# Performance work log

Hardware: AMD Instinct MI355X
Metric: run time of the kernel (lower is better)

Reference implementation:

```python
import jax, jax.numpy as jnp
import numpy as np
from jax import lax

V, E, H, N, To, Ti = 4000, 512, 512, 32, 128, 512
SOS_ID, EOS_ID = 1, 2


def setup_inputs() -> dict:
    key = jax.random.key(0)
    ks = jax.random.split(key, 16)
    s = 0.05
    inp = {}
    inp['padded_input'] = jax.random.randint(ks[0], (N, To), 0, V)
    inp['encoder_padded_outputs'] = jax.random.normal(ks[1], (N, Ti, H), dtype=jnp.float32)
    inp['embedding'] = jax.random.normal(ks[2], (V, E), dtype=jnp.float32) * s
    # LSTMCell layer 0: input = embedding_dim + encoder_hidden = E + H
    inp['W_ih0'] = jax.random.normal(ks[3], (4 * H, E + H), dtype=jnp.float32) * s
    inp['b_ih0'] = jnp.zeros((4 * H,), jnp.float32)
    inp['W_hh0'] = jax.random.normal(ks[4], (4 * H, H), dtype=jnp.float32) * s
    inp['b_hh0'] = jnp.zeros((4 * H,), jnp.float32)
    # LSTMCell layer 1: input = H
    inp['W_ih1'] = jax.random.normal(ks[5], (4 * H, H), dtype=jnp.float32) * s
    inp['b_ih1'] = jnp.zeros((4 * H,), jnp.float32)
    inp['W_hh1'] = jax.random.normal(ks[6], (4 * H, H), dtype=jnp.float32) * s
    inp['b_hh1'] = jnp.zeros((4 * H,), jnp.float32)
    # MLP: Linear(enc_hidden + hidden -> H), Tanh, Linear(H -> V)
    inp['W1'] = jax.random.normal(ks[7], (H, 2 * H), dtype=jnp.float32) * s
    inp['b1'] = jnp.zeros((H,), jnp.float32)
    inp['W2'] = jax.random.normal(ks[8], (V, H), dtype=jnp.float32) * s
    inp['b2'] = jnp.zeros((V,), jnp.float32)
    return inp


def _lstm_cell(x, h, c, W_ih, b_ih, W_hh, b_hh):
    g = x @ W_ih.T + b_ih + h @ W_hh.T + b_hh
    i, f, gg, o = jnp.split(g, 4, axis=-1)  # PyTorch gate order i,f,g,o
    c2 = jax.nn.sigmoid(f) * c + jax.nn.sigmoid(i) * jnp.tanh(gg)
    h2 = jax.nn.sigmoid(o) * jnp.tanh(c2)
    return h2, c2


def reference(padded_input, encoder_padded_outputs, embedding,
              W_ih0, b_ih0, W_hh0, b_hh0, W_ih1, b_ih1, W_hh1, b_hh1,
              W1, b1, W2, b2):
    n = padded_input.shape[0]
    sos = jnp.full((n, 1), SOS_ID, dtype=padded_input.dtype)
    eos = jnp.full((n, 1), EOS_ID, dtype=padded_input.dtype)
    ys_in = jnp.concatenate([sos, padded_input], axis=1)   # N x (To+1)
    ys_out = jnp.concatenate([padded_input, eos], axis=1)  # N x (To+1)
    T = ys_in.shape[1]

    emb = embedding[ys_in]  # N x T x E (teacher forcing path, sp == 0)
    enc = encoder_padded_outputs  # N x Ti x H

    def step(carry, x_t):
        h0, c0, h1, c1, att_c = carry
        rnn_in = jnp.concatenate([x_t, att_c], axis=-1)
        h0, c0 = _lstm_cell(rnn_in, h0, c0, W_ih0, b_ih0, W_hh0, b_hh0)
        h1, c1 = _lstm_cell(h0, h1, c1, W_ih1, b_ih1, W_hh1, b_hh1)
        # dot-product attention over encoder frames
        scores = jnp.einsum('nh,nth->nt', h1, enc)
        w = jax.nn.softmax(scores, axis=-1)
        att_c2 = jnp.einsum('nt,nth->nh', w, enc)
        mlp_in = jnp.concatenate([h1, att_c2], axis=-1)
        logits_t = jnp.tanh(mlp_in @ W1.T + b1) @ W2.T + b2  # N x V
        return (h0, c0, h1, c1, att_c2), logits_t

    z = jnp.zeros((n, H), jnp.float32)
    carry0 = (z, z, z, z, z)
    _, logits = lax.scan(step, carry0, jnp.swapaxes(emb, 0, 1))  # T x N x V
    logits = jnp.swapaxes(logits, 0, 1)  # N x T x V

    logp = jax.nn.log_softmax(logits, axis=-1)
    nll = -jnp.take_along_axis(logp, ys_out[..., None], axis=-1).squeeze(-1)
    ce = nll.mean()
    # torch path: ce *= mean(len(ys_in)) - 1 = (To+1) - 1 = T - 1
    return ce * (T - 1)
```

## Files before the change

kernel.cpp:

```cpp
#include <hip/hip_runtime.h>

typedef unsigned short us_t;
typedef unsigned int u32;
typedef unsigned long long u64;
typedef __attribute__((ext_vector_type(8))) short bf16x8;
typedef __attribute__((ext_vector_type(4))) float f32x4;

constexpr int V = 4000, E = 512, H = 512, NB = 32, To = 128, Ti = 512;
constexpr int T_STEPS = 129;

constexpr size_t OFF_XPRE = 0;
constexpr size_t OFF_WQ   = OFF_XPRE + (size_t)129*65536/2;
constexpr size_t OFF_WXP  = OFF_WQ + (size_t)256*128*16*8/2;
constexpr size_t OFF_W1P  = OFF_WXP + (size_t)64*2048*8/2;
constexpr size_t OFF_H0B  = OFF_W1P + (size_t)128*512*8/2;
constexpr size_t OFF_H1B  = OFF_H0B + (size_t)130*16384/2;
constexpr size_t OFF_H1T  = OFF_H1B + (size_t)130*16384/2;
constexpr size_t OFF_ATB  = OFF_H1T + (size_t)130*16640/2;
constexpr size_t OFF_CTX  = OFF_ATB + (size_t)130*16384/2;
constexpr size_t OFF_MZ   = OFF_CTX + (size_t)130*16384;
constexpr size_t OFF_HID  = OFF_MZ + (size_t)130*256*2;
constexpr size_t OFF_W2P  = OFF_HID + (size_t)4128*512/2;
constexpr size_t OFF_CPM  = OFF_W2P + (size_t)64*4096*8/2;
constexpr size_t OFF_CPS  = OFF_CPM + (size_t)4128*16;
constexpr size_t OFF_TGT  = OFF_CPS + (size_t)4128*16;
constexpr size_t OFF_FLG  = OFF_TGT + 4128;

__device__ __forceinline__ float sigmf(float x) { return 1.0f / (1.0f + __expf(-x)); }
__device__ __forceinline__ float tanh_fast(float x) {
    float e = __expf(-2.0f * fabsf(x));
    float t = (1.0f - e) / (1.0f + e);
    return copysignf(t, x);
}
__device__ __forceinline__ float bfl(u32 u) { return __uint_as_float(u << 16); }
__device__ __forceinline__ float bfh(u32 u) { return __uint_as_float(u & 0xffff0000u); }
__device__ __forceinline__ us_t f2b(float x) {
    u32 u = __float_as_uint(x);
    return (us_t)((u + 0x7fffu + ((u >> 16) & 1u)) >> 16);
}
__device__ __forceinline__ uint4 cvt_pk8(float4 a, float4 c) {
    u32 w0, w1, w2, w3;
    asm("v_cvt_pk_bf16_f32 %0, %1, %2" : "=v"(w0) : "v"(a.x), "v"(a.y));
    asm("v_cvt_pk_bf16_f32 %0, %1, %2" : "=v"(w1) : "v"(a.z), "v"(a.w));
    asm("v_cvt_pk_bf16_f32 %0, %1, %2" : "=v"(w2) : "v"(c.x), "v"(c.y));
    asm("v_cvt_pk_bf16_f32 %0, %1, %2" : "=v"(w3) : "v"(c.z), "v"(c.w));
    uint4 pk = {w0, w1, w2, w3};
    return pk;
}

__device__ __forceinline__ void arrive(u32* flg, int b, int tid, u32 val) {
    __syncthreads();
    if (tid == 0)
        __hip_atomic_store(flg + b, val, __ATOMIC_RELAXED, __HIP_MEMORY_SCOPE_AGENT);
}
__device__ __forceinline__ void wait_all(u32* flg, u32 target, int tid) {
    if (tid < 128) {
        const u64* f8 = (const u64*)flg;
        bool done = false;
        for (;;) {
            if (!done) {
                u64 v = __hip_atomic_load(f8 + tid, __ATOMIC_RELAXED, __HIP_MEMORY_SCOPE_AGENT);
                done = ((u32)v >= target) && ((u32)(v >> 32) >= target);
            }
            if (__all((int)done)) break;
            __builtin_amdgcn_s_sleep(2);
        }
    }
    __syncthreads();
}

__global__ __launch_bounds__(256) void k_init(float* ws) {
    int t0 = blockIdx.x * 256 + threadIdx.x;
    int nth = gridDim.x * 256;
    float4 z4 = {0.f, 0.f, 0.f, 0.f};
    float4* c4 = (float4*)(ws + OFF_CTX);
    for (int i = t0; i < 130 * 32 * 128; i += nth) c4[i] = z4;
    float4* m4 = (float4*)(ws + OFF_MZ);
    for (int i = t0; i < 130 * 128; i += nth) m4[i] = z4;
    float4* h04 = (float4*)(ws + OFF_H0B);
    float4* h14 = (float4*)(ws + OFF_H1B);
    for (int i = t0; i < 2048; i += nth) { h04[i] = z4; h14[i] = z4; }
    u32* fl = (u32*)(ws + OFF_FLG);
    if (t0 < 256) fl[t0] = 0u;
}

__global__ __launch_bounds__(256) void k_packWq(const float* __restrict__ W_ih0,
                                                const float* __restrict__ W_hh0,
                                                const float* __restrict__ W_ih1,
                                                const float* __restrict__ W_hh1,
                                                us_t* __restrict__ Wq) {
    int p = blockIdx.x * 256 + threadIdx.x;
    int j = p & 7, col = (p >> 3) & 15, r = (p >> 7) & 127, b = p >> 14;
    int k = r * 8 + j;
    int cl = col & 7;
    int gRow = (cl >> 1) * 512 + b * 2 + (cl & 1);
    float v;
    if (col < 8)
        v = (k < 512) ? W_ih0[(size_t)gRow * 1024 + 512 + k]
                      : W_hh0[(size_t)gRow * 512 + (k - 512)];
    else
        v = (k < 512) ? W_ih1[(size_t)gRow * 512 + k]
                      : W_hh1[(size_t)gRow * 512 + (k - 512)];
    Wq[p] = f2b(v);
}

__global__ __launch_bounds__(256) void k_packWx(const float* __restrict__ W_ih0,
                                                us_t* __restrict__ Wxp) {
    int p = blockIdx.x * 256 + threadIdx.x;
    int j = p & 7, g = (p >> 3) & 2047, kb = p >> 14;
    Wxp[p] = f2b(W_ih0[(size_t)g * 1024 + kb * 8 + j]);
}

__global__ __launch_bounds__(256) void k_packW1(const float* __restrict__ W1,
                                                us_t* __restrict__ W1p) {
    int p = blockIdx.x * 256 + threadIdx.x;
    int j = p & 7, c = (p >> 3) & 511, kb = p >> 12;
    W1p[p] = f2b(W1[(size_t)c * 1024 + kb * 8 + j]);
}

__global__ __launch_bounds__(256) void k_packW2(const float* __restrict__ W2,
                                                us_t* __restrict__ W2p) {
    int p = blockIdx.x * 256 + threadIdx.x;
    int j = p & 7, v = (p >> 3) & 4095, kb = p >> 15;
    float x = (v < V) ? W2[(size_t)v * 512 + kb * 8 + j] : 0.0f;
    W2p[p] = f2b(x);
}

__global__ __launch_bounds__(256) void k_xpre(const int* __restrict__ padded,
                                              const float* __restrict__ embedding,
                                              const us_t* __restrict__ Wxp,
                                              const float* __restrict__ b_ih0,
                                              const float* __restrict__ b_hh0,
                                              us_t* __restrict__ Xpre) {
    __shared__ __align__(16) us_t Ash[32 * 520];
    __shared__ int toks[32];
    const int t = blockIdx.x, gc = blockIdx.y, tid = threadIdx.x;
    if (tid < 32) toks[tid] = (t == 0) ? 1 : padded[tid * 128 + (t - 1)];
    __syncthreads();
#pragma unroll
    for (int i = 0; i < 16; ++i) {
        int f = tid + i * 256;
        int row = f >> 7, c4 = f & 127;
        float4 v = *(const float4*)(embedding + (size_t)toks[row] * 512 + c4 * 4);
        ushort4 o = {f2b(v.x), f2b(v.y), f2b(v.z), f2b(v.w)};
        *(ushort4*)(Ash + (size_t)row * 520 + c4 * 4) = o;
    }
    __syncthreads();
    const int w = tid >> 6, lane = tid & 63;
    const int quad = lane >> 4, l16 = lane & 15;
    f32x4 acc[2][4];
#pragma unroll
    for (int mt = 0; mt < 2; ++mt)
#pragma unroll
        for (int nt = 0; nt < 4; ++nt)
#pragma unroll
            for (int r = 0; r < 4; ++r) acc[mt][nt][r] = 0.0f;
    const int gbase = gc * 256 + w * 64;
    for (int ks = 0; ks < 16; ++ks) {
        bf16x8 a0 = *(const bf16x8*)(Ash + (size_t)(l16)      * 520 + ks * 32 + quad * 8);
        bf16x8 a1 = *(const bf16x8*)(Ash + (size_t)(16 + l16) * 520 + ks * 32 + quad * 8);
        const us_t* bp = Wxp + ((size_t)(ks * 4 + quad) * 2048 + gbase + l16) * 8;
#pragma unroll
        for (int nt = 0; nt < 4; ++nt) {
            bf16x8 bb = *(const bf16x8*)(bp + nt * 128);
            acc[0][nt] = __builtin_amdgcn_mfma_f32_16x16x32_bf16(a0, bb, acc[0][nt], 0, 0, 0);
            acc[1][nt] = __builtin_amdgcn_mfma_f32_16x16x32_bf16(a1, bb, acc[1][nt], 0, 0, 0);
        }
    }
    us_t* base = Xpre + (size_t)t * 65536;
#pragma unroll
    for (int nt = 0; nt < 4; ++nt) {
        int g = gc * 256 + w * 64 + nt * 16 + l16;
        float bias = b_ih0[g] + b_hh0[g];
#pragma unroll
        for (int mt = 0; mt < 2; ++mt) {
            ushort4 o = {f2b(acc[mt][nt][0] + bias), f2b(acc[mt][nt][1] + bias),
                         f2b(acc[mt][nt][2] + bias), f2b(acc[mt][nt][3] + bias)};
            *(ushort4*)(base + (size_t)g * 32 + mt * 16 + quad * 4) = o;
        }
    }
}

__device__ __forceinline__ void compute1(f32x4& a0, const us_t* __restrict__ Ab, int ktbase,
                                         int Mt, int kq, int l16, int quad,
                                         const us_t* __restrict__ lw) {
    bf16x8 av = *(const bf16x8*)(Ab + ((size_t)(kq * 4 + quad) * 32 + Mt * 16 + l16) * 8);
    bf16x8 bv = *(const bf16x8*)(lw + (((size_t)(ktbase + kq) * 4 + quad) * 16 + l16) * 8);
    a0 = __builtin_amdgcn_mfma_f32_16x16x32_bf16(av, bv, a0, 0, 0, 0);
}

__device__ __forceinline__ void tail_pub(f32x4 acc, int colbase,
                                         float g0, float g1, float g2, float g3,
                                         float& creg, u32* __restrict__ hOut32,
                                         u32* __restrict__ hT32,
                                         int b, int tid, float* red, float* gv) {
    const int l16 = tid & 15, quad = (tid >> 4) & 3, w = tid >> 6;
    const int Mt = w & 1, kq = w >> 1;
    const int cl = l16 - colbase;
    if ((unsigned)cl < 8u) {
        float4 v = {acc[0], acc[1], acc[2], acc[3]};
        *(float4*)&red[((size_t)(kq * 16 + Mt * 8 + cl)) * 20 + quad * 4] = v;
    }
    __syncthreads();
    if (tid < 256) {
        int row = tid >> 4, s = tid & 15;
        float g = 0.0f;
#pragma unroll
        for (int k2 = 0; k2 < 8; ++k2) g += red[((size_t)(k2 * 16 + row)) * 20 + s];
        gv[(row & 7) * 33 + (row >> 3) * 16 + s] = g;
    }
    __syncthreads();
    if (tid < 64) {
        int jl = tid >> 5, n = tid & 31;
        float gi = gv[jl * 33 + n]       + g0;
        float gf = gv[(2 + jl) * 33 + n] + g1;
        float gg = gv[(4 + jl) * 33 + n] + g2;
        float go = gv[(6 + jl) * 33 + n] + g3;
        float cn = sigmf(gf) * creg + sigmf(gi) * tanh_fast(gg);
        float hn = sigmf(go) * tanh_fast(cn);
        creg = cn;
        float hO = __shfl_xor(hn, 32);
        if (jl == 0) {
            u32 pk = (u32)f2b(hn) | ((u32)f2b(hO) << 16);
            __hip_atomic_store(hOut32 + (((size_t)(b >> 2) * 32 + n) * 4 + (b & 3)), pk,
                               __ATOMIC_RELAXED, __HIP_MEMORY_SCOPE_AGENT);
            if (hT32)
                __hip_atomic_store(hT32 + (n * 260 + b), pk,
                                   __ATOMIC_RELAXED, __HIP_MEMORY_SCOPE_AGENT);
        }
    }
}

__global__ __launch_bounds__(1024, 1) void k_seq(float* ws,
                                                 const float* __restrict__ enc,
                                                 const float* __restrict__ b_ih1,
                                                 const float* __restrict__ b_hh1) {
    __shared__ __align__(16) us_t lds_w[16384];
    __shared__ __align__(16) us_t lds_e[64 * 552];
    __shared__ __align__(16) us_t Ax[2][8192];
    __shared__ __align__(16) float red_s[8 * 16 * 20];
    __shared__ __align__(16) float gv_s[272];

    const int b = blockIdx.x, tid = threadIdx.x;
    const int w = tid >> 6, l16 = tid & 15, quad = (tid >> 4) & 3;
    const int Mt = w & 1, kq = w >> 1;
    us_t* Ax0 = Ax[0];
    us_t* Ax1 = Ax[1];

    const us_t* XpreB = (const us_t*)(ws + OFF_XPRE);
    us_t* h0b = (us_t*)(ws + OFF_H0B);
    us_t* h1b = (us_t*)(ws + OFF_H1B);
    u32*  h1T32 = (u32*)(ws + OFF_H1T);
    us_t* atb = (us_t*)(ws + OFF_ATB);
    float* ctx = ws + OFF_CTX;
    u64*  mz  = (u64*)(ws + OFF_MZ);
    u32* flg = (u32*)(ws + OFF_FLG);

    const int an = b & 31, ac = b >> 5;

    float c0r = 0.0f, c1r = 0.0f;

    float bs0 = 0.f, bs1 = 0.f, bs2 = 0.f, bs3 = 0.f;
    if (tid < 64) {
        int j = b * 2 + (tid >> 5);
        bs0 = b_ih1[j] + b_hh1[j];
        bs1 = b_ih1[512 + j] + b_hh1[512 + j];
        bs2 = b_ih1[1024 + j] + b_hh1[1024 + j];
        bs3 = b_ih1[1536 + j] + b_hh1[1536 + j];
    }

    {
        const uint4* wsrc = (const uint4*)((const us_t*)(ws + OFF_WQ) + (size_t)b * 16384);
        for (int f = tid; f < 2048; f += 1024) ((uint4*)lds_w)[f] = wsrc[f];
        const int ts0 = ac * 64;
        const float4* encn = (const float4*)(enc + ((size_t)an * 512 + ts0) * 512);
#pragma unroll
        for (int j = 0; j < 8; ++j) {
            int f = tid + j * 1024;
            int row = f >> 7, c4 = f & 127;
            float4 v = encn[(size_t)row * 128 + c4];
            ushort4 o;
            o.x = f2b(v.x); o.y = f2b(v.y); o.z = f2b(v.z); o.w = f2b(v.w);
            *(ushort4*)(lds_e + (size_t)row * 552 + (c4 >> 5) * 136 + (c4 & 31) * 4) = o;
        }
    }
    __syncthreads();

    for (int t = 0; t < T_STEPS; ++t) {
        const u32 base = 3u * t;
        float xg0 = 0.f, xg1 = 0.f, xg2 = 0.f, xg3 = 0.f;
        if (tid < 64) {
            const us_t* xp = XpreB + (size_t)t * 65536;
            int j = b * 2 + (tid >> 5), nn = tid & 31;
            xg0 = bfl(xp[(size_t)(0    + j) * 32 + nn]);
            xg1 = bfl(xp[(size_t)(512  + j) * 32 + nn]);
            xg2 = bfl(xp[(size_t)(1024 + j) * 32 + nn]);
            xg3 = bfl(xp[(size_t)(1536 + j) * 32 + nn]);
        }
        f32x4 acc;
#pragma unroll
        for (int r = 0; r < 4; ++r) acc[r] = 0.0f;
        {
            const us_t* h0s = h0b + (size_t)t * 16384;
            uint4 a0 = ((const uint4*)h0s)[tid];
            uint4 a1 = ((const uint4*)(h0s + 8192))[tid];
            ((uint4*)Ax0)[tid] = a0;
            __syncthreads();
            ((uint4*)Ax1)[tid] = a1;
            compute1(acc, Ax0, 16, Mt, kq, l16, quad, lds_w);
            __syncthreads();
            compute1(acc, Ax1, 24, Mt, kq, l16, quad, lds_w);
        }
        wait_all(flg, base, tid);
        {
            const float* cts = ctx + (size_t)t * 16384;
            us_t* atbt = atb + (size_t)t * 16384;
            float4 a0 = *(const float4*)(cts + (size_t)tid * 8);
            float4 c0 = *(const float4*)(cts + (size_t)tid * 8 + 4);
            float4 a1 = *(const float4*)(cts + (size_t)(1024 + tid) * 8);
            float4 c1 = *(const float4*)(cts + (size_t)(1024 + tid) * 8 + 4);
            uint4 pk0 = cvt_pk8(a0, c0);
            *(uint4*)(Ax0 + (size_t)tid * 8) = pk0;
            if ((tid >> 3) == b) *(uint4*)(atbt + (size_t)tid * 8) = pk0;
            __syncthreads();
            uint4 pk1 = cvt_pk8(a1, c1);
            *(uint4*)(Ax1 + (size_t)tid * 8) = pk1;
            {
                int gs = 1024 + tid;
                if ((gs >> 3) == b) *(uint4*)(atbt + (size_t)gs * 8) = pk1;
            }
            compute1(acc, Ax0, 0, Mt, kq, l16, quad, lds_w);
            __syncthreads();
            compute1(acc, Ax1, 8, Mt, kq, l16, quad, lds_w);
        }
        tail_pub(acc, 0, xg0, xg1, xg2, xg3, c0r,
                 (u32*)(h0b + (size_t)(t + 1) * 16384), nullptr, b, tid, red_s, gv_s);
        arrive(flg, b, tid, base + 1);
#pragma unroll
        for (int r = 0; r < 4; ++r) acc[r] = 0.0f;
        {
            const us_t* h1s = h1b + (size_t)t * 16384;
            uint4 a0 = ((const uint4*)h1s)[tid];
            uint4 a1 = ((const uint4*)(h1s + 8192))[tid];
            ((uint4*)Ax0)[tid] = a0;
            __syncthreads();
            ((uint4*)Ax1)[tid] = a1;
            compute1(acc, Ax0, 16, Mt, kq, l16, quad, lds_w);
            __syncthreads();
            compute1(acc, Ax1, 24, Mt, kq, l16, quad, lds_w);
        }
        wait_all(flg, base + 1, tid);
        {
            const us_t* h0n = h0b + (size_t)(t + 1) * 16384;
            uint4 a0 = ((const uint4*)h0n)[tid];
            uint4 a1 = ((const uint4*)(h0n + 8192))[tid];
            ((uint4*)Ax0)[tid] = a0;
            __syncthreads();
            ((uint4*)Ax1)[tid] = a1;
            compute1(acc, Ax0, 0, Mt, kq, l16, quad, lds_w);
            __syncthreads();
            compute1(acc, Ax1, 8, Mt, kq, l16, quad, lds_w);
        }
        tail_pub(acc, 8, bs0, bs1, bs2, bs3, c1r,
                 (u32*)(h1b + (size_t)(t + 1) * 16384),
                 h1T32 + (size_t)(t + 1) * 8320, b, tid, red_s, gv_s);
        arrive(flg, b, tid, base + 2);
        wait_all(flg, base + 2, tid);
        {
            float* h_l = (float*)Ax0;
            float* scp = h_l + 528;
            float* p_l = h_l + 1584;
            float* aux = h_l + 1648;
            if (tid < 256) {
                u32 hv = h1T32[(size_t)(t + 1) * 8320 + an * 260 + tid];
                int idx = tid * 2;
                int kp = idx >> 5, off = idx & 31;
                h_l[kp * 33 + off]     = bfl(hv);
                h_l[kp * 33 + off + 1] = bfh(hv);
            }
            __syncthreads();
            {
                int ti = tid >> 4, kp = tid & 15;
                const us_t* er = lds_e + (size_t)ti * 552 + (kp >> 2) * 136 + (kp & 3) * 32;
                const float* hr = h_l + kp * 33;
                float s = 0.0f;
#pragma unroll
                for (int k8 = 0; k8 < 4; ++k8) {
                    uint4 u = *(const uint4*)(er + k8 * 8);
                    const float* h8 = hr + k8 * 8;
                    s += bfl(u.x) * h8[0] + bfh(u.x) * h8[1]
                       + bfl(u.y) * h8[2] + bfh(u.y) * h8[3]
                       + bfl(u.z) * h8[4] + bfh(u.z) * h8[5]
                       + bfl(u.w) * h8[6] + bfh(u.w) * h8[7];
                }
                scp[kp * 66 + ti] = s;
            }
            __syncthreads();
            if (tid < 64) {
                float sc = 0.0f;
#pragma unroll
                for (int kp = 0; kp < 16; ++kp) sc += scp[kp * 66 + tid];
                float m = sc;
                for (int o = 32; o; o >>= 1) m = fmaxf(m, __shfl_xor(m, o));
                float e = __expf(sc - m);
                float z = e;
                for (int o = 32; o; o >>= 1) z += __shfl_xor(z, o);
                p_l[tid] = e;
                if (tid == 0) {
                    aux[0] = m;
                    u64 pk = ((u64)__float_as_uint(m) << 32) | (u64)__float_as_uint(z);
                    __hip_atomic_store(mz + ((size_t)(t + 1) * 256 + an * 8 + ac), pk,
                                       __ATOMIC_RELAXED, __HIP_MEMORY_SCOPE_AGENT);
                }
            }
            __syncthreads();
            int d = tid >> 1, half = tid & 1;
            const us_t* eb = lds_e + (d >> 7) * 136 + (d & 127);
            float cv = 0.0f;
#pragma unroll 8
            for (int i = 0; i < 32; ++i) {
                int ti2 = half * 32 + i;
                cv += p_l[ti2] * bfl((u32)eb[(size_t)ti2 * 552]);
            }
            if (tid < 8) {
                u64 v;
                for (;;) {
                    v = __hip_atomic_load(mz + ((size_t)(t + 1) * 256 + an * 8 + tid),
                                          __ATOMIC_RELAXED, __HIP_MEMORY_SCOPE_AGENT);
                    if ((u32)v != 0u) break;
                    __builtin_amdgcn_s_sleep(1);
                }
                float mi = __uint_as_float((u32)(v >> 32));
                float zi = __uint_as_float((u32)v);
#pragma unroll
                for (int o = 1; o < 8; o <<= 1) {
                    float mo = __shfl_xor(mi, o);
                    float zo = __shfl_xor(zi, o);
                    float Mn = fmaxf(mi, mo);
                    zi = zi * __expf(mi - Mn) + zo * __expf(mo - Mn);
                    mi = Mn;
                }
                if (tid == 0)
                    aux[1] = __expf(aux[0] - mi) / zi;
            }
            __syncthreads();
            float scl = aux[1];
            float ov = __shfl_xor(cv, 1);
            if (half == 0) {
                int gs = (d >> 3) * 32 + an;
                float* dst = ctx + (size_t)(t + 1) * 16384 + (size_t)gs * 8 + (d & 7);
                __hip_atomic_fetch_add(dst, (cv + ov) * scl,
                                       __ATOMIC_RELAXED, __HIP_MEMORY_SCOPE_AGENT);
            }
        }
        arrive(flg, b, tid, base + 3);
    }
    wait_all(flg, 3u * T_STEPS, tid);
    if (tid < 8) {
        int gs = b * 8 + tid;
        const float* s = ctx + (size_t)129 * 16384 + (size_t)gs * 8;
        float4 a = *(const float4*)s;
        float4 c = *(const float4*)(s + 4);
        uint4 pk = cvt_pk8(a, c);
        *(uint4*)(atb + (size_t)129 * 16384 + (size_t)gs * 8) = pk;
    }
}

__global__ __launch_bounds__(256) void k_mlp(const us_t* __restrict__ h1b,
                                             const us_t* __restrict__ atb,
                                             const us_t* __restrict__ W1p,
                                             const float* __restrict__ b1,
                                             us_t* __restrict__ hidb) {
    __shared__ __align__(16) us_t Ash[32 * 520];
    const int t = blockIdx.x, yc = blockIdx.y, tid = threadIdx.x;
    const int w = tid >> 6, lane = tid & 63;
    const int quad = lane >> 4, l16 = lane & 15;
    f32x4 acc[2][4];
#pragma unroll
    for (int mt = 0; mt < 2; ++mt)
#pragma unroll
        for (int nt = 0; nt < 4; ++nt)
#pragma unroll
            for (int r = 0; r < 4; ++r) acc[mt][nt][r] = 0.0f;
    const int cbase = yc * 256 + w * 64;
    for (int half = 0; half < 2; ++half) {
        const us_t* src = (half == 0) ? (h1b + (size_t)(t + 1) * 16384)
                                      : (atb + (size_t)t * 16384);
        __syncthreads();
#pragma unroll
        for (int i = 0; i < 8; ++i) {
            int f = tid + i * 256;
            int n = f & 31, g8 = f >> 5;
            uint4 v = *(const uint4*)(src + (size_t)f * 8);
            *(uint4*)(Ash + (size_t)n * 520 + g8 * 8) = v;
        }
        __syncthreads();
        for (int ks = 0; ks < 16; ++ks) {
            bf16x8 a0 = *(const bf16x8*)(Ash + (size_t)(l16)      * 520 + ks * 32 + quad * 8);
            bf16x8 a1 = *(const bf16x8*)(Ash + (size_t)(16 + l16) * 520 + ks * 32 + quad * 8);
            const us_t* bp = W1p + ((size_t)((half * 16 + ks) * 4 + quad) * 512 + cbase + l16) * 8;
#pragma unroll
            for (int nt = 0; nt < 4; ++nt) {
                bf16x8 bb = *(const bf16x8*)(bp + nt * 128);
                acc[0][nt] = __builtin_amdgcn_mfma_f32_16x16x32_bf16(a0, bb, acc[0][nt], 0, 0, 0);
                acc[1][nt] = __builtin_amdgcn_mfma_f32_16x16x32_bf16(a1, bb, acc[1][nt], 0, 0, 0);
            }
        }
    }
#pragma unroll
    for (int nt = 0; nt < 4; ++nt) {
        int c = yc * 256 + w * 64 + nt * 16 + l16;
        float bias = b1[c];
#pragma unroll
        for (int mt = 0; mt < 2; ++mt)
#pragma unroll
            for (int r = 0; r < 4; ++r) {
                int row = t * 32 + mt * 16 + quad * 4 + r;
                hidb[(size_t)row * 512 + c] = f2b(tanhf(acc[mt][nt][r] + bias));
            }
    }
}

__global__ __launch_bounds__(256) void k_ce(const us_t* __restrict__ hidb,
                                            const us_t* __restrict__ W2p,
                                            const float* __restrict__ b2,
                                            const int* __restrict__ padded,
                                            float* __restrict__ cpm, float* __restrict__ cps,
                                            float* __restrict__ tgt) {
    __shared__ __align__(16) us_t Ash[32 * 520];
    __shared__ __align__(16) float lg[256 * 33];
    __shared__ float mred[8 * 32];
    __shared__ float Mf[32];
    __shared__ float sred[8 * 32];
    const int t = blockIdx.x, vc = blockIdx.y, tid = threadIdx.x;
    {
        const uint4* src = (const uint4*)(hidb + (size_t)t * 32 * 512);
#pragma unroll
        for (int i = 0; i < 8; ++i) {
            int f = tid + i * 256;
            uint4 v = src[f];
            *(uint4*)(Ash + (size_t)(f >> 6) * 520 + (f & 63) * 8) = v;
        }
    }
    __syncthreads();
    const int w = tid >> 6, lane = tid & 63;
    const int quad = lane >> 4, l16 = lane & 15;
    f32x4 acc[2][4];
#pragma unroll
    for (int mt = 0; mt < 2; ++mt)
#pragma unroll
        for (int nt = 0; nt < 4; ++nt)
#pragma unroll
            for (int r = 0; r < 4; ++r) acc[mt][nt][r] = 0.0f;
    const int vbase = vc * 256 + w * 64;
    for (int ks = 0; ks < 16; ++ks) {
        bf16x8 a0 = *(const bf16x8*)(Ash + (size_t)(l16)      * 520 + ks * 32 + quad * 8);
        bf16x8 a1 = *(const bf16x8*)(Ash + (size_t)(16 + l16) * 520 + ks * 32 + quad * 8);
        const us_t* bp = W2p + ((size_t)(ks * 4 + quad) * 4096 + vbase + l16) * 8;
#pragma unroll
        for (int nt = 0; nt < 4; ++nt) {
            bf16x8 bb = *(const bf16x8*)(bp + nt * 128);
            acc[0][nt] = __builtin_amdgcn_mfma_f32_16x16x32_bf16(a0, bb, acc[0][nt], 0, 0, 0);
            acc[1][nt] = __builtin_amdgcn_mfma_f32_16x16x32_bf16(a1, bb, acc[1][nt], 0, 0, 0);
        }
    }
#pragma unroll
    for (int nt = 0; nt < 4; ++nt) {
        int vloc = w * 64 + nt * 16 + l16;
        int vglob = vc * 256 + vloc;
        float bias = (vglob < V) ? b2[vglob] : -1e30f;
#pragma unroll
        for (int mt = 0; mt < 2; ++mt)
#pragma unroll
            for (int r = 0; r < 4; ++r)
                lg[vloc * 33 + mt * 16 + quad * 4 + r] = acc[mt][nt][r] + bias;
    }
    __syncthreads();
    {
        int n = tid & 31, c = tid >> 5;
        float m = -1e30f;
        for (int i = 0; i < 32; ++i) m = fmaxf(m, lg[(c * 32 + i) * 33 + n]);
        mred[c * 32 + n] = m;
    }
    __syncthreads();
    if (tid < 32) {
        float M = mred[tid];
#pragma unroll
        for (int c = 1; c < 8; ++c) M = fmaxf(M, mred[c * 32 + tid]);
        Mf[tid] = M;
    }
    __syncthreads();
    {
        int n = tid & 31, c = tid >> 5;
        float M = Mf[n], s = 0.0f;
        for (int i = 0; i < 32; ++i) s += __expf(lg[(c * 32 + i) * 33 + n] - M);
        sred[c * 32 + n] = s;
    }
    __syncthreads();
    if (tid < 32) {
        int n = tid;
        float S = 0.0f;
#pragma unroll
        for (int c = 0; c < 8; ++c) S += sred[c * 32 + n];
        int r = t * 32 + n;
        cpm[(size_t)r * 16 + vc] = Mf[n];
        cps[(size_t)r * 16 + vc] = S;
        int vstar = (t < 128) ? padded[n * 128 + t] : 2;
        int vl = vstar - vc * 256;
        if (vl >= 0 && vl < 256) tgt[r] = lg[vl * 33 + n];
    }
}

__global__ __launch_bounds__(256) void k_final(const float* __restrict__ cpm,
                                               const float* __restrict__ cps,
                                               const float* __restrict__ tgt,
                                               float* __restrict__ out) {
    __shared__ float red[256];
    float local = 0.0f;
    for (int r = threadIdx.x; r < 4128; r += 256) {
        float M = -1e30f;
#pragma unroll
        for (int c = 0; c < 16; ++c) M = fmaxf(M, cpm[(size_t)r * 16 + c]);
        float S = 0.0f;
#pragma unroll
        for (int c = 0; c < 16; ++c) S += cps[(size_t)r * 16 + c] * __expf(cpm[(size_t)r * 16 + c] - M);
        local += (M + logf(S)) - tgt[r];
    }
    red[threadIdx.x] = local;
    __syncthreads();
    for (int o = 128; o; o >>= 1) {
        if (threadIdx.x < o) red[threadIdx.x] += red[threadIdx.x + o];
        __syncthreads();
    }
    if (threadIdx.x == 0) out[0] = red[0] * (128.0f / 4128.0f);
}

extern "C" void kernel_launch(void* const* d_in, const int* in_sizes, int n_in,
                              void* d_out, int out_size, void* d_ws, size_t ws_size,
                              hipStream_t stream) {
    const int*   padded = (const int*)d_in[0];
    const float* enc    = (const float*)d_in[1];
    const float* emb    = (const float*)d_in[2];
    const float* W_ih0  = (const float*)d_in[3];
    const float* b_ih0  = (const float*)d_in[4];
    const float* W_hh0  = (const float*)d_in[5];
    const float* b_hh0  = (const float*)d_in[6];
    const float* W_ih1  = (const float*)d_in[7];
    const float* b_ih1  = (const float*)d_in[8];
    const float* W_hh1  = (const float*)d_in[9];
    const float* b_hh1  = (const float*)d_in[10];
    const float* W1     = (const float*)d_in[11];
    const float* b1     = (const float*)d_in[12];
    const float* W2     = (const float*)d_in[13];
    const float* b2     = (const float*)d_in[14];
    float* ws  = (float*)d_ws;
    float* out = (float*)d_out;

    hipLaunchKernelGGL(k_init, dim3(640), dim3(256), 0, stream, ws);
    hipLaunchKernelGGL(k_packWq, dim3(16384), dim3(256), 0, stream,
                       W_ih0, W_hh0, W_ih1, W_hh1, (us_t*)(ws + OFF_WQ));
    hipLaunchKernelGGL(k_packWx, dim3(4096), dim3(256), 0, stream,
                       W_ih0, (us_t*)(ws + OFF_WXP));
    hipLaunchKernelGGL(k_packW1, dim3(2048), dim3(256), 0, stream,
                       W1, (us_t*)(ws + OFF_W1P));
    hipLaunchKernelGGL(k_packW2, dim3(8192), dim3(256), 0, stream,
                       W2, (us_t*)(ws + OFF_W2P));
    hipLaunchKernelGGL(k_xpre, dim3(129, 8), dim3(256), 0, stream,
                       padded, emb, (const us_t*)(ws + OFF_WXP), b_ih0, b_hh0,
                       (us_t*)(ws + OFF_XPRE));
    {
        float* ws_a = ws;
        const float* enc_a = enc;
        const float* bia = b_ih1;
        const float* bib = b_hh1;
        void* args[] = {(void*)&ws_a, (void*)&enc_a, (void*)&bia, (void*)&bib};
        hipLaunchCooperativeKernel((void*)k_seq, dim3(256), dim3(1024), args, 0, stream);
    }
    hipLaunchKernelGGL(k_mlp, dim3(129, 2), dim3(256), 0, stream,
                       (const us_t*)(ws + OFF_H1B), (const us_t*)(ws + OFF_ATB),
                       (const us_t*)(ws + OFF_W1P), b1, (us_t*)(ws + OFF_HID));
    hipLaunchKernelGGL(k_ce, dim3(129, 16), dim3(256), 0, stream,
                       (const us_t*)(ws + OFF_HID), (const us_t*)(ws + OFF_W2P), b2, padded,
                       ws + OFF_CPM, ws + OFF_CPS, ws + OFF_TGT);
    hipLaunchKernelGGL(k_final, dim3(1), dim3(256), 0, stream,
                       ws + OFF_CPM, ws + OFF_CPS, ws + OFF_TGT, out);
}
```

Before: 1.896 ms.

## Replace per-step grid barrier with tagged h1 publication; fuse pack kernels; register CE reductions

The h1 transposed buffer now stores 64-bit entries tagged with the step index. Attention blocks spin on the tag instead of a full grid-wide arrive/wait, which removes one global barrier per timestep. The four weight-pack kernels are merged into one launch. The CE kernel computes its max and sum reductions with wave shuffles in registers instead of staging logits in a large LDS array. The cost is doubled h1T storage and a larger zero-init, and correctness now depends on tags never colliding with stale values.

```diff
diff --git a/kernel.cpp b/kernel.cpp
--- a/kernel.cpp
+++ b/kernel.cpp
@@ -16,7 +16,7 @@
 constexpr size_t OFF_H0B  = OFF_W1P + (size_t)128*512*8/2;
 constexpr size_t OFF_H1B  = OFF_H0B + (size_t)130*16384/2;
 constexpr size_t OFF_H1T  = OFF_H1B + (size_t)130*16384/2;
-constexpr size_t OFF_ATB  = OFF_H1T + (size_t)130*16640/2;
+constexpr size_t OFF_ATB  = OFF_H1T + (size_t)130*8320*2;
 constexpr size_t OFF_CTX  = OFF_ATB + (size_t)130*16384/2;
 constexpr size_t OFF_MZ   = OFF_CTX + (size_t)130*16384;
 constexpr size_t OFF_HID  = OFF_MZ + (size_t)130*256*2;
@@ -47,6 +47,9 @@
     uint4 pk = {w0, w1, w2, w3};
     return pk;
 }
+__device__ __forceinline__ u64 aload64(const u64* p) {
+    return __hip_atomic_load(p, __ATOMIC_RELAXED, __HIP_MEMORY_SCOPE_AGENT);
+}
 
 __device__ __forceinline__ void arrive(u32* flg, int b, int tid, u32 val) {
     __syncthreads();
@@ -77,6 +80,8 @@
     for (int i = t0; i < 130 * 32 * 128; i += nth) c4[i] = z4;
     float4* m4 = (float4*)(ws + OFF_MZ);
     for (int i = t0; i < 130 * 128; i += nth) m4[i] = z4;
+    float4* t14 = (float4*)(ws + OFF_H1T);
+    for (int i = t0; i < 130 * 4160; i += nth) t14[i] = z4;
     float4* h04 = (float4*)(ws + OFF_H0B);
     float4* h14 = (float4*)(ws + OFF_H1B);
     for (int i = t0; i < 2048; i += nth) { h04[i] = z4; h14[i] = z4; }
@@ -84,46 +89,42 @@
     if (t0 < 256) fl[t0] = 0u;
 }
 
-__global__ __launch_bounds__(256) void k_packWq(const float* __restrict__ W_ih0,
-                                                const float* __restrict__ W_hh0,
-                                                const float* __restrict__ W_ih1,
-                                                const float* __restrict__ W_hh1,
-                                                us_t* __restrict__ Wq) {
-    int p = blockIdx.x * 256 + threadIdx.x;
-    int j = p & 7, col = (p >> 3) & 15, r = (p >> 7) & 127, b = p >> 14;
-    int k = r * 8 + j;
-    int cl = col & 7;
-    int gRow = (cl >> 1) * 512 + b * 2 + (cl & 1);
-    float v;
-    if (col < 8)
-        v = (k < 512) ? W_ih0[(size_t)gRow * 1024 + 512 + k]
-                      : W_hh0[(size_t)gRow * 512 + (k - 512)];
-    else
-        v = (k < 512) ? W_ih1[(size_t)gRow * 512 + k]
-                      : W_hh1[(size_t)gRow * 512 + (k - 512)];
-    Wq[p] = f2b(v);
-}
-
-__global__ __launch_bounds__(256) void k_packWx(const float* __restrict__ W_ih0,
-                                                us_t* __restrict__ Wxp) {
-    int p = blockIdx.x * 256 + threadIdx.x;
-    int j = p & 7, g = (p >> 3) & 2047, kb = p >> 14;
-    Wxp[p] = f2b(W_ih0[(size_t)g * 1024 + kb * 8 + j]);
-}
-
-__global__ __launch_bounds__(256) void k_packW1(const float* __restrict__ W1,
-                                                us_t* __restrict__ W1p) {
-    int p = blockIdx.x * 256 + threadIdx.x;
-    int j = p & 7, c = (p >> 3) & 511, kb = p >> 12;
-    W1p[p] = f2b(W1[(size_t)c * 1024 + kb * 8 + j]);
-}
-
-__global__ __launch_bounds__(256) void k_packW2(const float* __restrict__ W2,
-                                                us_t* __restrict__ W2p) {
-    int p = blockIdx.x * 256 + threadIdx.x;
-    int j = p & 7, v = (p >> 3) & 4095, kb = p >> 15;
-    float x = (v < V) ? W2[(size_t)v * 512 + kb * 8 + j] : 0.0f;
-    W2p[p] = f2b(x);
+__global__ __launch_bounds__(256) void k_pack(const float* __restrict__ W_ih0,
+                                              const float* __restrict__ W_hh0,
+                                              const float* __restrict__ W_ih1,
+                                              const float* __restrict__ W_hh1,
+                                              const float* __restrict__ W1,
+                                              const float* __restrict__ W2,
+                                              float* ws) {
+    int blk = blockIdx.x, tid = threadIdx.x;
+    if (blk < 16384) {
+        int p = blk * 256 + tid;
+        int j = p & 7, col = (p >> 3) & 15, r = (p >> 7) & 127, b = p >> 14;
+        int k = r * 8 + j;
+        int cl = col & 7;
+        int gRow = (cl >> 1) * 512 + b * 2 + (cl & 1);
+        float v;
+        if (col < 8)
+            v = (k < 512) ? W_ih0[(size_t)gRow * 1024 + 512 + k]
+                          : W_hh0[(size_t)gRow * 512 + (k - 512)];
+        else
+            v = (k < 512) ? W_ih1[(size_t)gRow * 512 + k]
+                          : W_hh1[(size_t)gRow * 512 + (k - 512)];
+        ((us_t*)(ws + OFF_WQ))[p] = f2b(v);
+    } else if (blk < 20480) {
+        int p = (blk - 16384) * 256 + tid;
+        int j = p & 7, g = (p >> 3) & 2047, kb = p >> 14;
+        ((us_t*)(ws + OFF_WXP))[p] = f2b(W_ih0[(size_t)g * 1024 + kb * 8 + j]);
+    } else if (blk < 22528) {
+        int p = (blk - 20480) * 256 + tid;
+        int j = p & 7, c = (p >> 3) & 511, kb = p >> 12;
+        ((us_t*)(ws + OFF_W1P))[p] = f2b(W1[(size_t)c * 1024 + kb * 8 + j]);
+    } else {
+        int p = (blk - 22528) * 256 + tid;
+        int j = p & 7, v = (p >> 3) & 4095, kb = p >> 15;
+        float x = (v < V) ? W2[(size_t)v * 512 + kb * 8 + j] : 0.0f;
+        ((us_t*)(ws + OFF_W2P))[p] = f2b(x);
+    }
 }
 
 __global__ __launch_bounds__(256) void k_xpre(const int* __restrict__ padded,
@@ -192,7 +193,7 @@
 __device__ __forceinline__ void tail_pub(f32x4 acc, int colbase,
                                          float g0, float g1, float g2, float g3,
                                          float& creg, u32* __restrict__ hOut32,
-                                         u32* __restrict__ hT32,
+                                         u64* __restrict__ tagT, u32 tag,
                                          int b, int tid, float* red, float* gv) {
     const int l16 = tid & 15, quad = (tid >> 4) & 3, w = tid >> 6;
     const int Mt = w & 1, kq = w >> 1;
@@ -224,9 +225,11 @@
             u32 pk = (u32)f2b(hn) | ((u32)f2b(hO) << 16);
             __hip_atomic_store(hOut32 + (((size_t)(b >> 2) * 32 + n) * 4 + (b & 3)), pk,
                                __ATOMIC_RELAXED, __HIP_MEMORY_SCOPE_AGENT);
-            if (hT32)
-                __hip_atomic_store(hT32 + (n * 260 + b), pk,
+            if (tagT) {
+                u64 pk64 = ((u64)tag << 32) | (u64)pk;
+                __hip_atomic_store(tagT + ((size_t)n * 260 + b), pk64,
                                    __ATOMIC_RELAXED, __HIP_MEMORY_SCOPE_AGENT);
+            }
         }
     }
 }
@@ -250,7 +253,7 @@
     const us_t* XpreB = (const us_t*)(ws + OFF_XPRE);
     us_t* h0b = (us_t*)(ws + OFF_H0B);
     us_t* h1b = (us_t*)(ws + OFF_H1B);
-    u32*  h1T32 = (u32*)(ws + OFF_H1T);
+    u64*  h1T = (u64*)(ws + OFF_H1T);
     us_t* atb = (us_t*)(ws + OFF_ATB);
     float* ctx = ws + OFF_CTX;
     u64*  mz  = (u64*)(ws + OFF_MZ);
@@ -287,7 +290,7 @@
     __syncthreads();
 
     for (int t = 0; t < T_STEPS; ++t) {
-        const u32 base = 3u * t;
+        const u32 base = 2u * t;
         float xg0 = 0.f, xg1 = 0.f, xg2 = 0.f, xg3 = 0.f;
         if (tid < 64) {
             const us_t* xp = XpreB + (size_t)t * 65536;
@@ -334,7 +337,7 @@
             compute1(acc, Ax1, 8, Mt, kq, l16, quad, lds_w);
         }
         tail_pub(acc, 0, xg0, xg1, xg2, xg3, c0r,
-                 (u32*)(h0b + (size_t)(t + 1) * 16384), nullptr, b, tid, red_s, gv_s);
+                 (u32*)(h0b + (size_t)(t + 1) * 16384), nullptr, 0u, b, tid, red_s, gv_s);
         arrive(flg, b, tid, base + 1);
 #pragma unroll
         for (int r = 0; r < 4; ++r) acc[r] = 0.0f;
@@ -363,16 +366,21 @@
         }
         tail_pub(acc, 8, bs0, bs1, bs2, bs3, c1r,
                  (u32*)(h1b + (size_t)(t + 1) * 16384),
-                 h1T32 + (size_t)(t + 1) * 8320, b, tid, red_s, gv_s);
-        arrive(flg, b, tid, base + 2);
-        wait_all(flg, base + 2, tid);
+                 h1T + (size_t)(t + 1) * 8320, (u32)(t + 1), b, tid, red_s, gv_s);
         {
             float* h_l = (float*)Ax0;
             float* scp = h_l + 528;
             float* p_l = h_l + 1584;
             float* aux = h_l + 1648;
             if (tid < 256) {
-                u32 hv = h1T32[(size_t)(t + 1) * 8320 + an * 260 + tid];
+                const u64* hp = h1T + (size_t)(t + 1) * 8320 + (size_t)an * 260 + tid;
+                u64 v;
+                for (;;) {
+                    v = aload64(hp);
+                    if ((u32)(v >> 32) == (u32)(t + 1)) break;
+                    __builtin_amdgcn_s_sleep(1);
+                }
+                u32 hv = (u32)v;
                 int idx = tid * 2;
                 int kp = idx >> 5, off = idx & 31;
                 h_l[kp * 33 + off]     = bfl(hv);
@@ -425,8 +433,7 @@
             if (tid < 8) {
                 u64 v;
                 for (;;) {
-                    v = __hip_atomic_load(mz + ((size_t)(t + 1) * 256 + an * 8 + tid),
-                                          __ATOMIC_RELAXED, __HIP_MEMORY_SCOPE_AGENT);
+                    v = aload64(mz + ((size_t)(t + 1) * 256 + an * 8 + tid));
                     if ((u32)v != 0u) break;
                     __builtin_amdgcn_s_sleep(1);
                 }
@@ -453,9 +460,9 @@
                                        __ATOMIC_RELAXED, __HIP_MEMORY_SCOPE_AGENT);
             }
         }
-        arrive(flg, b, tid, base + 3);
-    }
-    wait_all(flg, 3u * T_STEPS, tid);
+        arrive(flg, b, tid, base + 2);
+    }
+    wait_all(flg, 2u * T_STEPS, tid);
     if (tid < 8) {
         int gs = b * 8 + tid;
         const float* s = ctx + (size_t)129 * 16384 + (size_t)gs * 8;
@@ -528,11 +535,12 @@
                                             float* __restrict__ cpm, float* __restrict__ cps,
                                             float* __restrict__ tgt) {
     __shared__ __align__(16) us_t Ash[32 * 520];
-    __shared__ __align__(16) float lg[256 * 33];
-    __shared__ float mred[8 * 32];
+    __shared__ float mredL[4 * 32];
+    __shared__ float sredL[4 * 32];
     __shared__ float Mf[32];
-    __shared__ float sred[8 * 32];
+    __shared__ int svst[32];
     const int t = blockIdx.x, vc = blockIdx.y, tid = threadIdx.x;
+    if (tid < 32) svst[tid] = (t < 128) ? padded[tid * 128 + t] : 2;
     {
         const uint4* src = (const uint4*)(hidb + (size_t)t * 32 * 512);
 #pragma unroll
@@ -564,50 +572,77 @@
             acc[1][nt] = __builtin_amdgcn_mfma_f32_16x16x32_bf16(a1, bb, acc[1][nt], 0, 0, 0);
         }
     }
+    float bb4[4];
 #pragma unroll
     for (int nt = 0; nt < 4; ++nt) {
-        int vloc = w * 64 + nt * 16 + l16;
-        int vglob = vc * 256 + vloc;
-        float bias = (vglob < V) ? b2[vglob] : -1e30f;
+        int vg = vbase + nt * 16 + l16;
+        bb4[nt] = (vg < V) ? b2[vg] : -1e30f;
+    }
+    float lm[2][4];
+#pragma unroll
+    for (int mt = 0; mt < 2; ++mt)
+#pragma unroll
+        for (int r = 0; r < 4; ++r) {
+            float m = acc[mt][0][r] + bb4[0];
+            m = fmaxf(m, acc[mt][1][r] + bb4[1]);
+            m = fmaxf(m, acc[mt][2][r] + bb4[2]);
+            m = fmaxf(m, acc[mt][3][r] + bb4[3]);
+            lm[mt][r] = m;
+        }
+#pragma unroll
+    for (int o = 1; o < 16; o <<= 1)
 #pragma unroll
         for (int mt = 0; mt < 2; ++mt)
 #pragma unroll
             for (int r = 0; r < 4; ++r)
-                lg[vloc * 33 + mt * 16 + quad * 4 + r] = acc[mt][nt][r] + bias;
-    }
-    __syncthreads();
-    {
-        int n = tid & 31, c = tid >> 5;
-        float m = -1e30f;
-        for (int i = 0; i < 32; ++i) m = fmaxf(m, lg[(c * 32 + i) * 33 + n]);
-        mred[c * 32 + n] = m;
-    }
+                lm[mt][r] = fmaxf(lm[mt][r], __shfl_xor(lm[mt][r], o));
+    if (l16 == 0)
+#pragma unroll
+        for (int mt = 0; mt < 2; ++mt)
+#pragma unroll
+            for (int r = 0; r < 4; ++r)
+                mredL[w * 32 + mt * 16 + quad * 4 + r] = lm[mt][r];
+    __syncthreads();
+    if (tid < 32)
+        Mf[tid] = fmaxf(fmaxf(mredL[tid], mredL[32 + tid]),
+                        fmaxf(mredL[64 + tid], mredL[96 + tid]));
+    __syncthreads();
+    float sm[2][4];
+#pragma unroll
+    for (int mt = 0; mt < 2; ++mt)
+#pragma unroll
+        for (int r = 0; r < 4; ++r) {
+            int m = mt * 16 + quad * 4 + r;
+            float M = Mf[m];
+            int vsg = svst[m];
+            float s = 0.0f;
+#pragma unroll
+            for (int nt = 0; nt < 4; ++nt) {
+                float lv = acc[mt][nt][r] + bb4[nt];
+                s += __expf(lv - M);
+                if (vbase + nt * 16 + l16 == vsg) tgt[t * 32 + m] = lv;
+            }
+            sm[mt][r] = s;
+        }
+#pragma unroll
+    for (int o = 1; o < 16; o <<= 1)
+#pragma unroll
+        for (int mt = 0; mt < 2; ++mt)
+#pragma unroll
+            for (int r = 0; r < 4; ++r)
+                sm[mt][r] += __shfl_xor(sm[mt][r], o);
+    if (l16 == 0)
+#pragma unroll
+        for (int mt = 0; mt < 2; ++mt)
+#pragma unroll
+            for (int r = 0; r < 4; ++r)
+                sredL[w * 32 + mt * 16 + quad * 4 + r] = sm[mt][r];
     __syncthreads();
     if (tid < 32) {
-        float M = mred[tid];
-#pragma unroll
-        for (int c = 1; c < 8; ++c) M = fmaxf(M, mred[c * 32 + tid]);
-        Mf[tid] = M;
-    }
-    __syncthreads();
-    {
-        int n = tid & 31, c = tid >> 5;
-        float M = Mf[n], s = 0.0f;
-        for (int i = 0; i < 32; ++i) s += __expf(lg[(c * 32 + i) * 33 + n] - M);
-        sred[c * 32 + n] = s;
-    }
-    __syncthreads();
-    if (tid < 32) {
-        int n = tid;
-        float S = 0.0f;
-#pragma unroll
-        for (int c = 0; c < 8; ++c) S += sred[c * 32 + n];
-        int r = t * 32 + n;
-        cpm[(size_t)r * 16 + vc] = Mf[n];
+        float S = sredL[tid] + sredL[32 + tid] + sredL[64 + tid] + sredL[96 + tid];
+        int r = t * 32 + tid;
+        cpm[(size_t)r * 16 + vc] = Mf[tid];
         cps[(size_t)r * 16 + vc] = S;
-        int vstar = (t < 128) ? padded[n * 128 + t] : 2;
-        int vl = vstar - vc * 256;
-        if (vl >= 0 && vl < 256) tgt[r] = lg[vl * 33 + n];
     }
 }
 
@@ -657,14 +692,8 @@
     float* out = (float*)d_out;
 
     hipLaunchKernelGGL(k_init, dim3(640), dim3(256), 0, stream, ws);
-    hipLaunchKernelGGL(k_packWq, dim3(16384), dim3(256), 0, stream,
-                       W_ih0, W_hh0, W_ih1, W_hh1, (us_t*)(ws + OFF_WQ));
-    hipLaunchKernelGGL(k_packWx, dim3(4096), dim3(256), 0, stream,
-                       W_ih0, (us_t*)(ws + OFF_WXP));
-    hipLaunchKernelGGL(k_packW1, dim3(2048), dim3(256), 0, stream,
-                       W1, (us_t*)(ws + OFF_W1P));
-    hipLaunchKernelGGL(k_packW2, dim3(8192), dim3(256), 0, stream,
-                       W2, (us_t*)(ws + OFF_W2P));
+    hipLaunchKernelGGL(k_pack, dim3(30720), dim3(256), 0, stream,
+                       W_ih0, W_hh0, W_ih1, W_hh1, W1, W2, ws);
     hipLaunchKernelGGL(k_xpre, dim3(129, 8), dim3(256), 0, stream,
                        padded, emb, (const us_t*)(ws + OFF_WXP), b_ih0, b_hh0,
                        (us_t*)(ws + OFF_XPRE));
```

Measured after the change: 1.546 ms. -18.5%, faster.
